# Kernel tuning notes

Hardware: AMD Instinct MI355X
Metric: run time of the kernel (lower is better)

The kernel has to match this reference:

```python
import jax, jax.numpy as jnp
import numpy as np

# Hard-coded dims from the module: 76 subcarriers * 12 data OFDM symbols = 912 data REs,
# QPSK (2 bits/sym), rate 1/2 -> n=1824, k=912; 4 tx streams, 8 rx antennas.
B, S, K = 512, 4, 912      # batch, streams, info bits (= data REs per stream)
R = 8                       # rx antennas
D = K                       # data resource elements per stream
N_CODE = 2 * K              # coded bits
SH1, SH2 = 7, 150           # circulant shifts of the LDPC-like code
BP_ITERS = 10
INV_SQRT2 = 0.7071067811865476

# check c connects info vars {c, c-7, c-150 (mod K)} and parity var K+c -> check degree 4
_c = np.arange(K)
VAR_IDX = jnp.asarray(np.stack([_c % K, (_c - SH1) % K, (_c - SH2) % K, K + _c], axis=1), jnp.int32)  # [K,4]


def setup_inputs() -> dict:
    key = jax.random.key(0)
    k1, k2, k3, k4, k5 = jax.random.split(key, 5)
    return {
        "b_bits": jax.random.randint(k1, (B, S, K), 0, 2, dtype=jnp.int32),
        "h_real": jax.random.normal(k2, (B, D, R, S), dtype=jnp.float32),
        "h_imag": jax.random.normal(k3, (B, D, R, S), dtype=jnp.float32),
        "n_real": jax.random.normal(k4, (B, D, R), dtype=jnp.float32),
        "n_imag": jax.random.normal(k5, (B, D, R), dtype=jnp.float32),
        "ebno_db": 10,
    }


def _bp_decode(llr):
    """Min-sum BP decode. llr: [B,S,N_CODE] demapper LLRs (log p1/p0). Returns hard info bits."""
    L = (-llr).reshape(B * S, N_CODE)          # internal convention log(p0/p1)
    vflat = VAR_IDX.reshape(-1)
    c2v = jnp.zeros((B * S, K, 4), L.dtype)
    pos = jnp.arange(4)
    for _ in range(BP_ITERS):
        ext = jnp.zeros_like(L).at[:, vflat].add(c2v.reshape(B * S, -1))
        tot = L + ext
        m_vc = tot[:, VAR_IDX] - c2v           # [BS,K,4] var->check
        a = jnp.abs(m_vc)
        srt = jnp.sort(a, -1)
        min1, min2 = srt[..., 0:1], srt[..., 1:2]
        amin = jnp.argmin(a, -1, keepdims=True)
        excl = jnp.where(pos == amin, min2, min1)   # leave-one-out min
        s = jnp.where(m_vc < 0, -1.0, 1.0)
        s_excl = jnp.prod(s, -1, keepdims=True) * s  # sign product excluding self
        c2v = s_excl * excl
    ext = jnp.zeros_like(L).at[:, vflat].add(c2v.reshape(B * S, -1))
    tot = L + ext
    return (tot[:, :K] < 0).astype(jnp.int32).reshape(B, S, K)


def reference(b_bits, h_real, h_imag, n_real, n_imag, ebno_db):
    no = 10.0 ** (-float(ebno_db) / 10.0)  # ebnodb2no with 2 bits/sym * rate 1/2
    # --- LDPC-like systematic circulant encode: p = A b mod 2, c = [b | p] ---
    p = (b_bits + jnp.roll(b_bits, SH1, -1) + jnp.roll(b_bits, SH2, -1)) % 2
    c = jnp.concatenate([b_bits, p], -1)                    # [B,S,N_CODE]
    # --- Gray QPSK mapper ---
    cb = c.reshape(B, S, K, 2).astype(jnp.float32)
    x = ((1.0 - 2.0 * cb[..., 0]) + 1j * (1.0 - 2.0 * cb[..., 1])) * INV_SQRT2  # [B,S,D]
    x_rg = jnp.transpose(x, (0, 2, 1))                      # [B,D,S]
    # --- normalized Rayleigh MIMO channel per RE + AWGN ---
    h = ((h_real + 1j * h_imag) * INV_SQRT2).astype(jnp.complex64)  # [B,D,R,S], E|h|^2=1
    noise = (n_real + 1j * n_imag).astype(jnp.complex64) * np.float32(np.sqrt(no * 0.5))
    y = jnp.einsum('bdrs,bds->bdr', h, x_rg) + noise        # [B,D,R]
    # --- per-RE LMMSE equalizer with Sionna-style bias normalization ---
    hH = jnp.conj(jnp.swapaxes(h, -1, -2))                  # [B,D,S,R]
    A = jnp.einsum('bdsr,bdrt->bdst', hH, h) + jnp.asarray(no, h.dtype) * jnp.eye(S, dtype=h.dtype)
    G = jnp.linalg.solve(A, hH)                             # [B,D,S,R]
    z = jnp.einsum('bdsr,bdr->bds', G, y)
    dgg = jnp.clip(jnp.real(jnp.einsum('bdsr,bdrs->bds', G, h)), 1e-6, 1.0 - 1e-6)
    x_hat = z / dgg.astype(jnp.complex64)
    no_eff = (1.0 - dgg) / dgg                              # [B,D,S]
    # --- exact APP QPSK demapper: llr = log p1/p0 ---
    scale = -2.0 * np.float32(np.sqrt(2.0)) / no_eff
    llr = jnp.stack([scale * jnp.real(x_hat), scale * jnp.imag(x_hat)], -1)  # [B,D,S,2]
    llr = jnp.transpose(llr, (0, 2, 1, 3)).reshape(B, S, N_CODE)
    # --- BP decode ---
    b_hat = _bp_decode(llr)
    return b_bits, b_hat
```

## Files before the change

### kernel.cpp

```cpp
#include <hip/hip_runtime.h>

#define B_ 512
#define S_ 4
#define K_ 912
#define R_ 8
#define D_ 912
#define NCODE 1824
#define BSK (B_*S_*K_)
#define BP_ITERS 10
#define NTH 228

__global__ void setup_kernel(const int* __restrict__ ebno, float* __restrict__ cst) {
  int ei = ebno[0];
  float ef = (ei >= -100 && ei <= 100) ? (float)ei : __int_as_float(ei);
  double no_d = pow(10.0, -(double)ef / 10.0);
  cst[0] = (float)no_d;
  cst[1] = (float)sqrt(no_d * 0.5);
}

__global__ __launch_bounds__(256) void mmse_llr_kernel(
    const int* __restrict__ bbits, const float* __restrict__ hre,
    const float* __restrict__ him, const float* __restrict__ nre,
    const float* __restrict__ nim, const float* __restrict__ cst,
    float* __restrict__ outf) {
#pragma clang fp contract(off)
  __shared__ float4 shre[1024];
  __shared__ float4 shim[1024];
  int tid = threadIdx.x;
  int t0 = blockIdx.x * 256;
  int t = t0 + tid;
  int b = t / D_;
  int d = t - b * D_;

  const float no_f = cst[0];
  const float nscale = cst[1];
  const float INV2 = 0.70710678118654752440f;

  float xr[S_], xq[S_];
  int k2 = 2 * d;
#pragma unroll
  for (int s = 0; s < S_; ++s) {
    const int* bb = bbits + (b * S_ + s) * K_;
    int c0, c1;
    if (k2 < K_) {
      c0 = bb[k2];
      c1 = bb[k2 + 1];
    } else {
      int j0 = k2 - K_, j1 = k2 + 1 - K_;
      int j0a = j0 - 7;   if (j0a < 0) j0a += K_;
      int j0b = j0 - 150; if (j0b < 0) j0b += K_;
      c0 = (bb[j0] + bb[j0a] + bb[j0b]) & 1;
      int j1a = j1 - 7;   if (j1a < 0) j1a += K_;
      int j1b = j1 - 150; if (j1b < 0) j1b += K_;
      c1 = (bb[j1] + bb[j1a] + bb[j1b]) & 1;
    }
    xr[s] = (1.0f - 2.0f * (float)c0) * INV2;
    xq[s] = (1.0f - 2.0f * (float)c1) * INV2;
  }

  const float4* nr4 = reinterpret_cast<const float4*>(nre + (size_t)t * 8);
  const float4* ni4 = reinterpret_cast<const float4*>(nim + (size_t)t * 8);
  float nrv[8], niv[8];
  {
    float4 a = nr4[0], b2 = nr4[1];
    nrv[0]=a.x; nrv[1]=a.y; nrv[2]=a.z; nrv[3]=a.w;
    nrv[4]=b2.x; nrv[5]=b2.y; nrv[6]=b2.z; nrv[7]=b2.w;
    float4 c = ni4[0], d2 = ni4[1];
    niv[0]=c.x; niv[1]=c.y; niv[2]=c.z; niv[3]=c.w;
    niv[4]=d2.x; niv[5]=d2.y; niv[6]=d2.z; niv[7]=d2.w;
  }

  const float4* hre4 = reinterpret_cast<const float4*>(hre);
  const float4* him4 = reinterpret_cast<const float4*>(him);

  float Ad0=0.f, Ad1=0.f, Ad2=0.f, Ad3=0.f;
  float A10r=0.f,A10i=0.f,A20r=0.f,A20i=0.f,A21r=0.f,A21i=0.f;
  float A30r=0.f,A30i=0.f,A31r=0.f,A31i=0.f,A32r=0.f,A32i=0.f;
  float w0r=0.f,w0i=0.f,w1r=0.f,w1i=0.f,w2r=0.f,w2i=0.f,w3r=0.f,w3i=0.f;

#pragma unroll
  for (int half = 0; half < 2; ++half) {
    if (half) __syncthreads();
#pragma unroll
    for (int j = 0; j < 4; ++j) {
      int m = j * 256 + tid;
      int T = m >> 2, q = m & 3;
      size_t gidx = (size_t)(t0 + T) * 8 + half * 4 + q;
      float4 vr = hre4[gidx];
      float4 vi = him4[gidx];
      int dst = T * 4 + (q ^ ((T >> 1) & 3));
      shre[dst] = vr;
      shim[dst] = vi;
    }
    __syncthreads();
#pragma unroll
    for (int rr = 0; rr < 4; ++rr) {
      int r = half * 4 + rr;
      int slot = rr ^ ((tid >> 1) & 3);
      float4 h4r = shre[tid * 4 + slot];
      float4 h4i = shim[tid * 4 + slot];
      float hr0=h4r.x*INV2, hr1=h4r.y*INV2, hr2=h4r.z*INV2, hr3=h4r.w*INV2;
      float hi0=h4i.x*INV2, hi1=h4i.y*INV2, hi2=h4i.z*INV2, hi3=h4i.w*INV2;
      float yr = 0.f, yi = 0.f;
      yr += hr0*xr[0] - hi0*xq[0]; yi += hr0*xq[0] + hi0*xr[0];
      yr += hr1*xr[1] - hi1*xq[1]; yi += hr1*xq[1] + hi1*xr[1];
      yr += hr2*xr[2] - hi2*xq[2]; yi += hr2*xq[2] + hi2*xr[2];
      yr += hr3*xr[3] - hi3*xq[3]; yi += hr3*xq[3] + hi3*xr[3];
      yr += nrv[r]*nscale; yi += niv[r]*nscale;
      Ad0 += hr0*hr0 + hi0*hi0;
      Ad1 += hr1*hr1 + hi1*hi1;
      Ad2 += hr2*hr2 + hi2*hi2;
      Ad3 += hr3*hr3 + hi3*hi3;
      A10r += hr1*hr0 + hi1*hi0;  A10i += hr1*hi0 - hi1*hr0;
      A20r += hr2*hr0 + hi2*hi0;  A20i += hr2*hi0 - hi2*hr0;
      A21r += hr2*hr1 + hi2*hi1;  A21i += hr2*hi1 - hi2*hr1;
      A30r += hr3*hr0 + hi3*hi0;  A30i += hr3*hi0 - hi3*hr0;
      A31r += hr3*hr1 + hi3*hi1;  A31i += hr3*hi1 - hi3*hr1;
      A32r += hr3*hr2 + hi3*hi2;  A32i += hr3*hi2 - hi3*hr2;
      w0r += hr0*yr + hi0*yi;  w0i += hr0*yi - hi0*yr;
      w1r += hr1*yr + hi1*yi;  w1i += hr1*yi - hi1*yr;
      w2r += hr2*yr + hi2*yi;  w2i += hr2*yi - hi2*yr;
      w3r += hr3*yr + hi3*yi;  w3i += hr3*yi - hi3*yr;
    }
  }

  float Dv0 = Ad0 + no_f;
  float iD0 = 1.0f / Dv0;
  float L10r = A10r*iD0, L10i = A10i*iD0;
  float L20r = A20r*iD0, L20i = A20i*iD0;
  float L30r = A30r*iD0, L30i = A30i*iD0;
  float Dv1 = Ad1 + no_f - (L10r*L10r + L10i*L10i)*Dv0;
  float iD1 = 1.0f / Dv1;
  float t21r = A21r - (L20r*L10r + L20i*L10i)*Dv0;
  float t21i = A21i - (L20i*L10r - L20r*L10i)*Dv0;
  float L21r = t21r*iD1, L21i = t21i*iD1;
  float t31r = A31r - (L30r*L10r + L30i*L10i)*Dv0;
  float t31i = A31i - (L30i*L10r - L30r*L10i)*Dv0;
  float L31r = t31r*iD1, L31i = t31i*iD1;
  float Dv2 = Ad2 + no_f - (L20r*L20r + L20i*L20i)*Dv0 - (L21r*L21r + L21i*L21i)*Dv1;
  float iD2 = 1.0f / Dv2;
  float t32r = A32r - (L30r*L20r + L30i*L20i)*Dv0 - (L31r*L21r + L31i*L21i)*Dv1;
  float t32i = A32i - (L30i*L20r - L30r*L20i)*Dv0 - (L31i*L21r - L31r*L21i)*Dv1;
  float L32r = t32r*iD2, L32i = t32i*iD2;
  float Dv3 = Ad3 + no_f - (L30r*L30r + L30i*L30i)*Dv0 - (L31r*L31r + L31i*L31i)*Dv1
                        - (L32r*L32r + L32i*L32i)*Dv2;
  float iD3 = 1.0f / Dv3;

  float c0r = w0r, c0i = w0i;
  float c1r = w1r - (L10r*c0r - L10i*c0i);
  float c1i = w1i - (L10r*c0i + L10i*c0r);
  float c2r = w2r - (L20r*c0r - L20i*c0i) - (L21r*c1r - L21i*c1i);
  float c2i = w2i - (L20r*c0i + L20i*c0r) - (L21r*c1i + L21i*c1r);
  float c3r = w3r - (L30r*c0r - L30i*c0i) - (L31r*c1r - L31i*c1i) - (L32r*c2r - L32i*c2i);
  float c3i = w3i - (L30r*c0i + L30i*c0r) - (L31r*c1i + L31i*c1r) - (L32r*c2i + L32i*c2r);
  c0r *= iD0; c0i *= iD0;
  c1r *= iD1; c1i *= iD1;
  c2r *= iD2; c2i *= iD2;
  c3r *= iD3; c3i *= iD3;
  float z3r = c3r, z3i = c3i;
  float z2r = c2r - (L32r*z3r + L32i*z3i);
  float z2i = c2i - (L32r*z3i - L32i*z3r);
  float z1r = c1r - (L21r*z2r + L21i*z2i) - (L31r*z3r + L31i*z3i);
  float z1i = c1i - (L21r*z2i - L21i*z2r) - (L31r*z3i - L31i*z3r);
  float z0r = c0r - (L10r*z1r + L10i*z1i) - (L20r*z2r + L20i*z2i) - (L30r*z3r + L30i*z3i);
  float z0i = c0i - (L10r*z1i - L10i*z1r) - (L20r*z2i - L20i*z2r) - (L30r*z3i - L30i*z3r);

  float M10r = -L10r, M10i = -L10i;
  float M21r = -L21r, M21i = -L21i;
  float M32r = -L32r, M32i = -L32i;
  float M20r = -L20r - (L21r*M10r - L21i*M10i);
  float M20i = -L20i - (L21r*M10i + L21i*M10r);
  float M31r = -L31r - (L32r*M21r - L32i*M21i);
  float M31i = -L31i - (L32r*M21i + L32i*M21r);
  float M30r = -L30r - (L31r*M10r - L31i*M10i) - (L32r*M20r - L32i*M20i);
  float M30i = -L30i - (L31r*M10i + L31i*M10r) - (L32r*M20i + L32i*M20r);
  float Ai0 = iD0 + (M10r*M10r + M10i*M10i)*iD1 + (M20r*M20r + M20i*M20i)*iD2
                  + (M30r*M30r + M30i*M30i)*iD3;
  float Ai1 = iD1 + (M21r*M21r + M21i*M21i)*iD2 + (M31r*M31r + M31i*M31i)*iD3;
  float Ai2 = iD2 + (M32r*M32r + M32i*M32i)*iD3;
  float Ai3 = iD3;

  float zrv[4] = {z0r, z1r, z2r, z3r};
  float ziv[4] = {z0i, z1i, z2i, z3i};
  float Aiv[4] = {Ai0, Ai1, Ai2, Ai3};

#pragma unroll
  for (int s = 0; s < S_; ++s) {
    float dgg = 1.0f - no_f * Aiv[s];
    float dg = fminf(fmaxf(dgg, 1e-6f), (float)(1.0 - 1e-6));
    float xhr = zrv[s] / dg;
    float xhi = ziv[s] / dg;
    float noe = (1.0f - dg) / dg;
    float sc = -2.8284270763397217f / noe;
    float2 o;
    o.x = -(sc * xhr);
    o.y = -(sc * xhi);
    size_t w = (size_t)(b * S_ + s);
    if (k2 < K_) {
      *reinterpret_cast<float2*>(outf + w * K_ + k2) = o;
    } else {
      *reinterpret_cast<float2*>(outf + (size_t)BSK + w * K_ + (k2 - K_)) = o;
    }
  }
}

__global__ __launch_bounds__(256) void bp_kernel(const int* __restrict__ bbits,
                                                 int* __restrict__ out) {
#pragma clang fp contract(off)
  __shared__ float tot[K_];
  __shared__ float E0[K_];
  __shared__ float E1[K_];
  __shared__ float E2[K_];
  int w = blockIdx.x;
  int tid = threadIdx.x;
  const float* outf = (const float*)out;
  bool act = tid < NTH;

  float Lv[4], LP[4];
  float c0v[4] = {0.f,0.f,0.f,0.f};
  float c1v[4] = {0.f,0.f,0.f,0.f};
  float c2v_[4] = {0.f,0.f,0.f,0.f};
  float c3v[4] = {0.f,0.f,0.f,0.f};

  if (act) {
#pragma unroll
    for (int k = 0; k < 4; ++k) {
      int n = tid + NTH * k;
      Lv[k] = outf[(size_t)w * K_ + n];
      LP[k] = outf[(size_t)BSK + (size_t)w * K_ + n];
      E0[n] = 0.f; E1[n] = 0.f; E2[n] = 0.f;
    }
  }
  __syncthreads();

  for (int it = 0; it < BP_ITERS; ++it) {
    if (act) {
#pragma unroll
      for (int k = 0; k < 4; ++k) {
        int n = tid + NTH * k;
        tot[n] = Lv[k] + ((E0[n] + E1[n]) + E2[n]);
      }
    }
    __syncthreads();
    if (act) {
#pragma unroll
      for (int k = 0; k < 4; ++k) {
        int c = tid + NTH * k;
        int i1 = c - 7;   if (i1 < 0) i1 += K_;
        int i2 = c - 150; if (i2 < 0) i2 += K_;
        float m0 = tot[c]  - c0v[k];
        float m1 = tot[i1] - c1v[k];
        float m2 = tot[i2] - c2v_[k];
        float totP = LP[k] + c3v[k];
        float m3 = totP - c3v[k];
        float a0 = fabsf(m0), a1 = fabsf(m1), a2 = fabsf(m2), a3 = fabsf(m3);
        float t01 = fminf(a0, a1), t23 = fminf(a2, a3);
        float e0 = fminf(a1, t23);
        float e1 = fminf(a0, t23);
        float e2 = fminf(t01, a3);
        float e3 = fminf(t01, a2);
        unsigned s0 = __float_as_uint(m0) & 0x80000000u;
        unsigned s1 = __float_as_uint(m1) & 0x80000000u;
        unsigned s2 = __float_as_uint(m2) & 0x80000000u;
        unsigned s3 = __float_as_uint(m3) & 0x80000000u;
        unsigned sp = (s0 ^ s1) ^ (s2 ^ s3);
        float n0 = __uint_as_float(__float_as_uint(e0) ^ (sp ^ s0));
        float n1 = __uint_as_float(__float_as_uint(e1) ^ (sp ^ s1));
        float n2 = __uint_as_float(__float_as_uint(e2) ^ (sp ^ s2));
        float n3 = __uint_as_float(__float_as_uint(e3) ^ (sp ^ s3));
        c0v[k] = n0; c1v[k] = n1; c2v_[k] = n2; c3v[k] = n3;
        E0[c] = n0; E1[i1] = n1; E2[i2] = n2;
      }
    }
    __syncthreads();
  }

  if (act) {
#pragma unroll
    for (int k = 0; k < 4; ++k) {
      int n = tid + NTH * k;
      float ttt = Lv[k] + ((E0[n] + E1[n]) + E2[n]);
      out[(size_t)BSK + (size_t)w * K_ + n] = (ttt < 0.f) ? 1 : 0;
      out[(size_t)w * K_ + n] = bbits[(size_t)w * K_ + n];
    }
  }
}

extern "C" void kernel_launch(void* const* d_in, const int* in_sizes, int n_in,
                              void* d_out, int out_size, void* d_ws, size_t ws_size,
                              hipStream_t stream) {
  const int*   b_bits = (const int*)d_in[0];
  const float* h_real = (const float*)d_in[1];
  const float* h_imag = (const float*)d_in[2];
  const float* n_real = (const float*)d_in[3];
  const float* n_imag = (const float*)d_in[4];
  const int*   ebno   = (const int*)d_in[5];
  int* out = (int*)d_out;
  float* cst = (float*)d_ws;

  setup_kernel<<<1, 1, 0, stream>>>(ebno, cst);
  mmse_llr_kernel<<<(B_ * D_) / 256, 256, 0, stream>>>(
      b_bits, h_real, h_imag, n_real, n_imag, cst, (float*)d_out);
  bp_kernel<<<B_ * S_, 256, 0, stream>>>(b_bits, out);
}
```

Baseline: 67.92 us.

## Assign one thread per rx antenna and reduce Gram terms via shuffles

The MMSE kernel now uses 8 threads per resource element, one per receive antenna. Each thread loads its float4 of channel coefficients directly with coalesced reads, and the 24 Gram and matched-filter accumulators are summed with xor-shuffle butterflies. This removes the shared-memory staging, the swizzle and the barriers, and raises parallelism 8x. In exchange, the Cholesky solve and the bit/codeword fetch are repeated in all 8 lanes, and only one lane writes output, so redundant ALU and load work grows.

```diff
diff --git a/kernel.cpp b/kernel.cpp
--- a/kernel.cpp
+++ b/kernel.cpp
@@ -18,19 +18,19 @@
   cst[1] = (float)sqrt(no_d * 0.5);
 }
 
+#define BFLY(v) { v += __shfl_xor(v, 1); v += __shfl_xor(v, 2); v += __shfl_xor(v, 4); }
+
 __global__ __launch_bounds__(256) void mmse_llr_kernel(
     const int* __restrict__ bbits, const float* __restrict__ hre,
     const float* __restrict__ him, const float* __restrict__ nre,
     const float* __restrict__ nim, const float* __restrict__ cst,
     float* __restrict__ outf) {
 #pragma clang fp contract(off)
-  __shared__ float4 shre[1024];
-  __shared__ float4 shim[1024];
-  int tid = threadIdx.x;
-  int t0 = blockIdx.x * 256;
-  int t = t0 + tid;
-  int b = t / D_;
-  int d = t - b * D_;
+  int t = blockIdx.x * 256 + threadIdx.x;
+  int g = t >> 3;
+  int r = t & 7;
+  int b = g / D_;
+  int d = g - b * D_;
 
   const float no_f = cst[0];
   const float nscale = cst[1];
@@ -58,71 +58,39 @@
     xq[s] = (1.0f - 2.0f * (float)c1) * INV2;
   }
 
-  const float4* nr4 = reinterpret_cast<const float4*>(nre + (size_t)t * 8);
-  const float4* ni4 = reinterpret_cast<const float4*>(nim + (size_t)t * 8);
-  float nrv[8], niv[8];
-  {
-    float4 a = nr4[0], b2 = nr4[1];
-    nrv[0]=a.x; nrv[1]=a.y; nrv[2]=a.z; nrv[3]=a.w;
-    nrv[4]=b2.x; nrv[5]=b2.y; nrv[6]=b2.z; nrv[7]=b2.w;
-    float4 c = ni4[0], d2 = ni4[1];
-    niv[0]=c.x; niv[1]=c.y; niv[2]=c.z; niv[3]=c.w;
-    niv[4]=d2.x; niv[5]=d2.y; niv[6]=d2.z; niv[7]=d2.w;
-  }
-
-  const float4* hre4 = reinterpret_cast<const float4*>(hre);
-  const float4* him4 = reinterpret_cast<const float4*>(him);
-
-  float Ad0=0.f, Ad1=0.f, Ad2=0.f, Ad3=0.f;
-  float A10r=0.f,A10i=0.f,A20r=0.f,A20i=0.f,A21r=0.f,A21i=0.f;
-  float A30r=0.f,A30i=0.f,A31r=0.f,A31i=0.f,A32r=0.f,A32i=0.f;
-  float w0r=0.f,w0i=0.f,w1r=0.f,w1i=0.f,w2r=0.f,w2i=0.f,w3r=0.f,w3i=0.f;
-
-#pragma unroll
-  for (int half = 0; half < 2; ++half) {
-    if (half) __syncthreads();
-#pragma unroll
-    for (int j = 0; j < 4; ++j) {
-      int m = j * 256 + tid;
-      int T = m >> 2, q = m & 3;
-      size_t gidx = (size_t)(t0 + T) * 8 + half * 4 + q;
-      float4 vr = hre4[gidx];
-      float4 vi = him4[gidx];
-      int dst = T * 4 + (q ^ ((T >> 1) & 3));
-      shre[dst] = vr;
-      shim[dst] = vi;
-    }
-    __syncthreads();
-#pragma unroll
-    for (int rr = 0; rr < 4; ++rr) {
-      int r = half * 4 + rr;
-      int slot = rr ^ ((tid >> 1) & 3);
-      float4 h4r = shre[tid * 4 + slot];
-      float4 h4i = shim[tid * 4 + slot];
-      float hr0=h4r.x*INV2, hr1=h4r.y*INV2, hr2=h4r.z*INV2, hr3=h4r.w*INV2;
-      float hi0=h4i.x*INV2, hi1=h4i.y*INV2, hi2=h4i.z*INV2, hi3=h4i.w*INV2;
-      float yr = 0.f, yi = 0.f;
-      yr += hr0*xr[0] - hi0*xq[0]; yi += hr0*xq[0] + hi0*xr[0];
-      yr += hr1*xr[1] - hi1*xq[1]; yi += hr1*xq[1] + hi1*xr[1];
-      yr += hr2*xr[2] - hi2*xq[2]; yi += hr2*xq[2] + hi2*xr[2];
-      yr += hr3*xr[3] - hi3*xq[3]; yi += hr3*xq[3] + hi3*xr[3];
-      yr += nrv[r]*nscale; yi += niv[r]*nscale;
-      Ad0 += hr0*hr0 + hi0*hi0;
-      Ad1 += hr1*hr1 + hi1*hi1;
-      Ad2 += hr2*hr2 + hi2*hi2;
-      Ad3 += hr3*hr3 + hi3*hi3;
-      A10r += hr1*hr0 + hi1*hi0;  A10i += hr1*hi0 - hi1*hr0;
-      A20r += hr2*hr0 + hi2*hi0;  A20i += hr2*hi0 - hi2*hr0;
-      A21r += hr2*hr1 + hi2*hi1;  A21i += hr2*hi1 - hi2*hr1;
-      A30r += hr3*hr0 + hi3*hi0;  A30i += hr3*hi0 - hi3*hr0;
-      A31r += hr3*hr1 + hi3*hi1;  A31i += hr3*hi1 - hi3*hr1;
-      A32r += hr3*hr2 + hi3*hi2;  A32i += hr3*hi2 - hi3*hr2;
-      w0r += hr0*yr + hi0*yi;  w0i += hr0*yi - hi0*yr;
-      w1r += hr1*yr + hi1*yi;  w1i += hr1*yi - hi1*yr;
-      w2r += hr2*yr + hi2*yi;  w2i += hr2*yi - hi2*yr;
-      w3r += hr3*yr + hi3*yi;  w3i += hr3*yi - hi3*yr;
-    }
-  }
+  float4 h4r = reinterpret_cast<const float4*>(hre)[t];
+  float4 h4i = reinterpret_cast<const float4*>(him)[t];
+  float hr0=h4r.x*INV2, hr1=h4r.y*INV2, hr2=h4r.z*INV2, hr3=h4r.w*INV2;
+  float hi0=h4i.x*INV2, hi1=h4i.y*INV2, hi2=h4i.z*INV2, hi3=h4i.w*INV2;
+
+  float yr = 0.f, yi = 0.f;
+  yr += hr0*xr[0] - hi0*xq[0]; yi += hr0*xq[0] + hi0*xr[0];
+  yr += hr1*xr[1] - hi1*xq[1]; yi += hr1*xq[1] + hi1*xr[1];
+  yr += hr2*xr[2] - hi2*xq[2]; yi += hr2*xq[2] + hi2*xr[2];
+  yr += hr3*xr[3] - hi3*xq[3]; yi += hr3*xq[3] + hi3*xr[3];
+  yr += nre[t] * nscale;
+  yi += nim[t] * nscale;
+
+  float Ad0 = hr0*hr0 + hi0*hi0;
+  float Ad1 = hr1*hr1 + hi1*hi1;
+  float Ad2 = hr2*hr2 + hi2*hi2;
+  float Ad3 = hr3*hr3 + hi3*hi3;
+  float A10r = hr1*hr0 + hi1*hi0, A10i = hr1*hi0 - hi1*hr0;
+  float A20r = hr2*hr0 + hi2*hi0, A20i = hr2*hi0 - hi2*hr0;
+  float A21r = hr2*hr1 + hi2*hi1, A21i = hr2*hi1 - hi2*hr1;
+  float A30r = hr3*hr0 + hi3*hi0, A30i = hr3*hi0 - hi3*hr0;
+  float A31r = hr3*hr1 + hi3*hi1, A31i = hr3*hi1 - hi3*hr1;
+  float A32r = hr3*hr2 + hi3*hi2, A32i = hr3*hi2 - hi3*hr2;
+  float w0r = hr0*yr + hi0*yi, w0i = hr0*yi - hi0*yr;
+  float w1r = hr1*yr + hi1*yi, w1i = hr1*yi - hi1*yr;
+  float w2r = hr2*yr + hi2*yi, w2i = hr2*yi - hi2*yr;
+  float w3r = hr3*yr + hi3*yi, w3i = hr3*yi - hi3*yr;
+
+  BFLY(Ad0) BFLY(Ad1) BFLY(Ad2) BFLY(Ad3)
+  BFLY(A10r) BFLY(A10i) BFLY(A20r) BFLY(A20i) BFLY(A21r) BFLY(A21i)
+  BFLY(A30r) BFLY(A30i) BFLY(A31r) BFLY(A31i) BFLY(A32r) BFLY(A32i)
+  BFLY(w0r) BFLY(w0i) BFLY(w1r) BFLY(w1i)
+  BFLY(w2r) BFLY(w2i) BFLY(w3r) BFLY(w3i)
 
   float Dv0 = Ad0 + no_f;
   float iD0 = 1.0f / Dv0;
@@ -180,26 +148,27 @@
   float Ai2 = iD2 + (M32r*M32r + M32i*M32i)*iD3;
   float Ai3 = iD3;
 
-  float zrv[4] = {z0r, z1r, z2r, z3r};
-  float ziv[4] = {z0i, z1i, z2i, z3i};
-  float Aiv[4] = {Ai0, Ai1, Ai2, Ai3};
-
-#pragma unroll
-  for (int s = 0; s < S_; ++s) {
-    float dgg = 1.0f - no_f * Aiv[s];
-    float dg = fminf(fmaxf(dgg, 1e-6f), (float)(1.0 - 1e-6));
-    float xhr = zrv[s] / dg;
-    float xhi = ziv[s] / dg;
-    float noe = (1.0f - dg) / dg;
-    float sc = -2.8284270763397217f / noe;
-    float2 o;
-    o.x = -(sc * xhr);
-    o.y = -(sc * xhi);
-    size_t w = (size_t)(b * S_ + s);
-    if (k2 < K_) {
-      *reinterpret_cast<float2*>(outf + w * K_ + k2) = o;
-    } else {
-      *reinterpret_cast<float2*>(outf + (size_t)BSK + w * K_ + (k2 - K_)) = o;
+  if (r == 0) {
+    float zrv[4] = {z0r, z1r, z2r, z3r};
+    float ziv[4] = {z0i, z1i, z2i, z3i};
+    float Aiv[4] = {Ai0, Ai1, Ai2, Ai3};
+#pragma unroll
+    for (int s = 0; s < S_; ++s) {
+      float dgg = 1.0f - no_f * Aiv[s];
+      float dg = fminf(fmaxf(dgg, 1e-6f), (float)(1.0 - 1e-6));
+      float xhr = zrv[s] / dg;
+      float xhi = ziv[s] / dg;
+      float noe = (1.0f - dg) / dg;
+      float sc = -2.8284270763397217f / noe;
+      float2 o;
+      o.x = -(sc * xhr);
+      o.y = -(sc * xhi);
+      size_t w = (size_t)(b * S_ + s);
+      if (k2 < K_) {
+        *reinterpret_cast<float2*>(outf + w * K_ + k2) = o;
+      } else {
+        *reinterpret_cast<float2*>(outf + (size_t)BSK + w * K_ + (k2 - K_)) = o;
+      }
     }
   }
 }
@@ -299,7 +268,7 @@
   float* cst = (float*)d_ws;
 
   setup_kernel<<<1, 1, 0, stream>>>(ebno, cst);
-  mmse_llr_kernel<<<(B_ * D_) / 256, 256, 0, stream>>>(
+  mmse_llr_kernel<<<(B_ * D_ * 8) / 256, 256, 0, stream>>>(
       b_bits, h_real, h_imag, n_real, n_imag, cst, (float*)d_out);
   bp_kernel<<<B_ * S_, 256, 0, stream>>>(b_bits, out);
 }
```

Result: slower. 102.0 us (+50.1%).

## Split each RE across two threads with shuffle reduction, drop LDS staging

Applied to the files above, without the earlier changes.

Each resource element is now handled by two adjacent lanes, each covering four of the eight receive antennas. Partial Gram and matched-filter sums are combined with a lane-xor shuffle, and each lane writes LLRs for two streams. This removes the shared-memory transpose and barriers in favour of direct float4 loads, and doubles the number of threads to hide memory latency. In exchange the Cholesky/inverse math is computed redundantly in both lanes, and global loads are less contiguous per lane.

```diff
diff --git a/kernel.cpp b/kernel.cpp
--- a/kernel.cpp
+++ b/kernel.cpp
@@ -18,19 +18,19 @@
   cst[1] = (float)sqrt(no_d * 0.5);
 }
 
+#define BFLY1(v) { v += __shfl_xor(v, 1); }
+
 __global__ __launch_bounds__(256) void mmse_llr_kernel(
     const int* __restrict__ bbits, const float* __restrict__ hre,
     const float* __restrict__ him, const float* __restrict__ nre,
     const float* __restrict__ nim, const float* __restrict__ cst,
     float* __restrict__ outf) {
 #pragma clang fp contract(off)
-  __shared__ float4 shre[1024];
-  __shared__ float4 shim[1024];
-  int tid = threadIdx.x;
-  int t0 = blockIdx.x * 256;
-  int t = t0 + tid;
-  int b = t / D_;
-  int d = t - b * D_;
+  int t = blockIdx.x * 256 + threadIdx.x;
+  int g = t >> 1;
+  int half = t & 1;
+  int b = g / D_;
+  int d = g - b * D_;
 
   const float no_f = cst[0];
   const float nscale = cst[1];
@@ -58,17 +58,10 @@
     xq[s] = (1.0f - 2.0f * (float)c1) * INV2;
   }
 
-  const float4* nr4 = reinterpret_cast<const float4*>(nre + (size_t)t * 8);
-  const float4* ni4 = reinterpret_cast<const float4*>(nim + (size_t)t * 8);
-  float nrv[8], niv[8];
-  {
-    float4 a = nr4[0], b2 = nr4[1];
-    nrv[0]=a.x; nrv[1]=a.y; nrv[2]=a.z; nrv[3]=a.w;
-    nrv[4]=b2.x; nrv[5]=b2.y; nrv[6]=b2.z; nrv[7]=b2.w;
-    float4 c = ni4[0], d2 = ni4[1];
-    niv[0]=c.x; niv[1]=c.y; niv[2]=c.z; niv[3]=c.w;
-    niv[4]=d2.x; niv[5]=d2.y; niv[6]=d2.z; niv[7]=d2.w;
-  }
+  float4 nr4v = reinterpret_cast<const float4*>(nre)[t];
+  float4 ni4v = reinterpret_cast<const float4*>(nim)[t];
+  float nrv[4] = {nr4v.x, nr4v.y, nr4v.z, nr4v.w};
+  float niv[4] = {ni4v.x, ni4v.y, ni4v.z, ni4v.w};
 
   const float4* hre4 = reinterpret_cast<const float4*>(hre);
   const float4* him4 = reinterpret_cast<const float4*>(him);
@@ -79,50 +72,38 @@
   float w0r=0.f,w0i=0.f,w1r=0.f,w1i=0.f,w2r=0.f,w2i=0.f,w3r=0.f,w3i=0.f;
 
 #pragma unroll
-  for (int half = 0; half < 2; ++half) {
-    if (half) __syncthreads();
-#pragma unroll
-    for (int j = 0; j < 4; ++j) {
-      int m = j * 256 + tid;
-      int T = m >> 2, q = m & 3;
-      size_t gidx = (size_t)(t0 + T) * 8 + half * 4 + q;
-      float4 vr = hre4[gidx];
-      float4 vi = him4[gidx];
-      int dst = T * 4 + (q ^ ((T >> 1) & 3));
-      shre[dst] = vr;
-      shim[dst] = vi;
-    }
-    __syncthreads();
-#pragma unroll
-    for (int rr = 0; rr < 4; ++rr) {
-      int r = half * 4 + rr;
-      int slot = rr ^ ((tid >> 1) & 3);
-      float4 h4r = shre[tid * 4 + slot];
-      float4 h4i = shim[tid * 4 + slot];
-      float hr0=h4r.x*INV2, hr1=h4r.y*INV2, hr2=h4r.z*INV2, hr3=h4r.w*INV2;
-      float hi0=h4i.x*INV2, hi1=h4i.y*INV2, hi2=h4i.z*INV2, hi3=h4i.w*INV2;
-      float yr = 0.f, yi = 0.f;
-      yr += hr0*xr[0] - hi0*xq[0]; yi += hr0*xq[0] + hi0*xr[0];
-      yr += hr1*xr[1] - hi1*xq[1]; yi += hr1*xq[1] + hi1*xr[1];
-      yr += hr2*xr[2] - hi2*xq[2]; yi += hr2*xq[2] + hi2*xr[2];
-      yr += hr3*xr[3] - hi3*xq[3]; yi += hr3*xq[3] + hi3*xr[3];
-      yr += nrv[r]*nscale; yi += niv[r]*nscale;
-      Ad0 += hr0*hr0 + hi0*hi0;
-      Ad1 += hr1*hr1 + hi1*hi1;
-      Ad2 += hr2*hr2 + hi2*hi2;
-      Ad3 += hr3*hr3 + hi3*hi3;
-      A10r += hr1*hr0 + hi1*hi0;  A10i += hr1*hi0 - hi1*hr0;
-      A20r += hr2*hr0 + hi2*hi0;  A20i += hr2*hi0 - hi2*hr0;
-      A21r += hr2*hr1 + hi2*hi1;  A21i += hr2*hi1 - hi2*hr1;
-      A30r += hr3*hr0 + hi3*hi0;  A30i += hr3*hi0 - hi3*hr0;
-      A31r += hr3*hr1 + hi3*hi1;  A31i += hr3*hi1 - hi3*hr1;
-      A32r += hr3*hr2 + hi3*hi2;  A32i += hr3*hi2 - hi3*hr2;
-      w0r += hr0*yr + hi0*yi;  w0i += hr0*yi - hi0*yr;
-      w1r += hr1*yr + hi1*yi;  w1i += hr1*yi - hi1*yr;
-      w2r += hr2*yr + hi2*yi;  w2i += hr2*yi - hi2*yr;
-      w3r += hr3*yr + hi3*yi;  w3i += hr3*yi - hi3*yr;
-    }
-  }
+  for (int q = 0; q < 4; ++q) {
+    float4 h4r = hre4[(size_t)t * 4 + q];
+    float4 h4i = him4[(size_t)t * 4 + q];
+    float hr0=h4r.x*INV2, hr1=h4r.y*INV2, hr2=h4r.z*INV2, hr3=h4r.w*INV2;
+    float hi0=h4i.x*INV2, hi1=h4i.y*INV2, hi2=h4i.z*INV2, hi3=h4i.w*INV2;
+    float yr = 0.f, yi = 0.f;
+    yr += hr0*xr[0] - hi0*xq[0]; yi += hr0*xq[0] + hi0*xr[0];
+    yr += hr1*xr[1] - hi1*xq[1]; yi += hr1*xq[1] + hi1*xr[1];
+    yr += hr2*xr[2] - hi2*xq[2]; yi += hr2*xq[2] + hi2*xr[2];
+    yr += hr3*xr[3] - hi3*xq[3]; yi += hr3*xq[3] + hi3*xr[3];
+    yr += nrv[q]*nscale; yi += niv[q]*nscale;
+    Ad0 += hr0*hr0 + hi0*hi0;
+    Ad1 += hr1*hr1 + hi1*hi1;
+    Ad2 += hr2*hr2 + hi2*hi2;
+    Ad3 += hr3*hr3 + hi3*hi3;
+    A10r += hr1*hr0 + hi1*hi0;  A10i += hr1*hi0 - hi1*hr0;
+    A20r += hr2*hr0 + hi2*hi0;  A20i += hr2*hi0 - hi2*hr0;
+    A21r += hr2*hr1 + hi2*hi1;  A21i += hr2*hi1 - hi2*hr1;
+    A30r += hr3*hr0 + hi3*hi0;  A30i += hr3*hi0 - hi3*hr0;
+    A31r += hr3*hr1 + hi3*hi1;  A31i += hr3*hi1 - hi3*hr1;
+    A32r += hr3*hr2 + hi3*hi2;  A32i += hr3*hi2 - hi3*hr2;
+    w0r += hr0*yr + hi0*yi;  w0i += hr0*yi - hi0*yr;
+    w1r += hr1*yr + hi1*yi;  w1i += hr1*yi - hi1*yr;
+    w2r += hr2*yr + hi2*yi;  w2i += hr2*yi - hi2*yr;
+    w3r += hr3*yr + hi3*yi;  w3i += hr3*yi - hi3*yr;
+  }
+
+  BFLY1(Ad0) BFLY1(Ad1) BFLY1(Ad2) BFLY1(Ad3)
+  BFLY1(A10r) BFLY1(A10i) BFLY1(A20r) BFLY1(A20i) BFLY1(A21r) BFLY1(A21i)
+  BFLY1(A30r) BFLY1(A30i) BFLY1(A31r) BFLY1(A31i) BFLY1(A32r) BFLY1(A32i)
+  BFLY1(w0r) BFLY1(w0i) BFLY1(w1r) BFLY1(w1i)
+  BFLY1(w2r) BFLY1(w2i) BFLY1(w3r) BFLY1(w3i)
 
   float Dv0 = Ad0 + no_f;
   float iD0 = 1.0f / Dv0;
@@ -185,7 +166,8 @@
   float Aiv[4] = {Ai0, Ai1, Ai2, Ai3};
 
 #pragma unroll
-  for (int s = 0; s < S_; ++s) {
+  for (int j = 0; j < 2; ++j) {
+    int s = half * 2 + j;
     float dgg = 1.0f - no_f * Aiv[s];
     float dg = fminf(fmaxf(dgg, 1e-6f), (float)(1.0 - 1e-6));
     float xhr = zrv[s] / dg;
@@ -299,7 +281,7 @@
   float* cst = (float*)d_ws;
 
   setup_kernel<<<1, 1, 0, stream>>>(ebno, cst);
-  mmse_llr_kernel<<<(B_ * D_) / 256, 256, 0, stream>>>(
+  mmse_llr_kernel<<<(B_ * D_ * 2) / 256, 256, 0, stream>>>(
       b_bits, h_real, h_imag, n_real, n_imag, cst, (float*)d_out);
   bp_kernel<<<B_ * S_, 256, 0, stream>>>(b_bits, out);
 }
```

New measurement: 61.17 us (median of 2 runs). 9.9% less time.
